# Kernel optimization log

Hardware: AMD Instinct MI355X
Metric: run time of the kernel (lower is better)

The kernel has to match this reference:

```python
import jax, jax.numpy as jnp
import numpy as np

DIM = 16      # sdefunc.dim (latent channels)
S = 64        # spatial side of latent volume
HID = 64      # drift conv hidden channels
DT = 0.05     # sdeint dt
SIGMA = 0.1   # diagonal diffusion coefficient
N_STEPS = 20  # (t1 - t0) / dt with ts = [0, 1]


def conv3d(v, w, b):
    # v: [B, C, D, H, W], w: [O, I, 3, 3, 3]
    y = jax.lax.conv_general_dilated(
        v, w, window_strides=(1, 1, 1), padding='SAME',
        dimension_numbers=('NCDHW', 'OIDHW', 'NCDHW'))
    return y + b[None, :, None, None, None]


def setup_inputs() -> dict:
    key = jax.random.key(0)
    k = jax.random.split(key, 6)
    x = jax.random.normal(k[0], (1, DIM, S, S, S), dtype=jnp.float32)
    integration_time = jnp.arange(2, dtype=jnp.float32)  # ts = [0.0, 1.0]
    # drift network params (Conv3d(DIM->HID) -> tanh -> Conv3d(HID->DIM))
    w1 = jax.random.normal(k[1], (HID, DIM, 3, 3, 3), dtype=jnp.float32) / np.sqrt(DIM * 27)
    b1 = jnp.zeros((HID,), dtype=jnp.float32)
    w2 = jax.random.normal(k[2], (DIM, HID, 3, 3, 3), dtype=jnp.float32) / np.sqrt(HID * 27)
    b2 = jnp.zeros((DIM,), dtype=jnp.float32)
    # pre-sampled standard-normal Brownian increments, one per Euler step
    noise = jax.random.normal(k[3], (N_STEPS, 1, DIM * S * S * S), dtype=jnp.float32)
    return {"x": x, "integration_time": integration_time,
            "w1": w1, "b1": b1, "w2": w2, "b2": b2, "noise": noise}


def reference(x, integration_time, w1, b1, w2, b2, noise):
    B = x.shape[0]  # == 1 (required by the original reshape)
    y0 = x.reshape(B, -1)  # [B, DIM*S^3]
    sqrt_dt = jnp.float32(DT ** 0.5)

    def drift(y):
        v = y.reshape(B, DIM, S, S, S)
        h = jnp.tanh(conv3d(v, w1, b1))
        f = conv3d(h, w2, b2)
        return f.reshape(B, -1)

    def step(y, z):
        # Euler-Maruyama, diagonal noise: y += f(t,y) dt + sigma * sqrt(dt) * z
        y = y + drift(y) * DT + SIGMA * sqrt_dt * z
        return y, None

    yT, _ = jax.lax.scan(step, y0, noise)
    out = yT.reshape(DIM, S, S, S)  # out[-1] of the trajectory (B == 1)
    return out[None]  # [1, DIM, S, S, S]
```

## Files before the change

### kernel.cpp

```cpp
#include <hip/hip_runtime.h>
#include <hip/hip_bf16.h>


#define S    64
#define SS   4096
#define SSS  262144
#define DT_F 0.05f
#define SIG_SDT 0.022360679774997897f

typedef __bf16 bf16x8 __attribute__((ext_vector_type(8)));
typedef float  f32x4  __attribute__((ext_vector_type(4)));
typedef float  f32x16 __attribute__((ext_vector_type(16)));

union B8U { uint4 u; bf16x8 b; };
__device__ inline bf16x8 as_bf16x8(uint4 u) { B8U x; x.u = u; return x.b; }

__device__ inline unsigned short bf16_bits(float f) {
    union { float f; unsigned u; } c; c.f = f;
    unsigned r = c.u + 0x7fffu + ((c.u >> 16) & 1u);
    return (unsigned short)(r >> 16);
}

__device__ inline float tanh_fast(float v) {
    float a = fminf(fmaxf(v, -15.f), 15.f);
    float e = __expf(2.f * a);
    return (e - 1.f) * __builtin_amdgcn_rcpf(e + 1.f);
}

__global__ void prep_weights(const float* __restrict__ w1, const float* __restrict__ w2,
                             unsigned short* __restrict__ w1t, unsigned short* __restrict__ w2t)
{
    const int t = blockIdx.x * 256 + threadIdx.x;
    if (t >= 27 * 2 * 64 * 8) return;
    const int j = t & 7, l = (t >> 3) & 63, half = (t >> 9) & 1, tap = t >> 10;
    {
        const int oc = half * 32 + (l & 31), ic = (l >> 5) * 8 + j;
        w1t[t] = bf16_bits(w1[(oc * 16 + ic) * 27 + tap]);
    }
    {
        const int oc = l & 15, ic = half * 32 + (l >> 4) * 8 + j;
        w2t[t] = bf16_bits(w2[(oc * 64 + ic) * 27 + tap]);
    }
}

__global__ void pack_x(const float* __restrict__ x, uint4* __restrict__ yb)
{
    const int p = blockIdx.x * 256 + threadIdx.x;
    union { unsigned short s[16]; uint4 v[2]; } pk;
    #pragma unroll
    for (int c = 0; c < 16; ++c) pk.s[c] = bf16_bits(x[c * SSS + p]);
    yb[p * 2]     = pk.v[0];
    yb[p * 2 + 1] = pk.v[1];
}

__device__ inline void stage1(const uint4* __restrict__ yb, uint4* tile,
                              int y, int zp, int t)
{
    uint4* dst = tile + ((zp % 3 + 3) % 3) * 396;
    for (int idx = t; idx < 396; idx += 256) {
        const int r = idx / 132, rem = idx - r * 132;
        const int px = rem >> 1;
        const int gy = y + r - 1, gx = px - 1;
        uint4 v = {0, 0, 0, 0};
        if ((unsigned)zp < 64u && (unsigned)gy < 64u && (unsigned)gx < 64u)
            v = yb[(((size_t)zp * SS + gy * S + gx) << 1) + (rem & 1)];
        dst[idx] = v;
    }
}

__global__ __launch_bounds__(256, 2)
void conv1_mfma(const uint4* __restrict__ yb, const uint4* __restrict__ w1t,
                const float* __restrict__ b1, unsigned short* __restrict__ h)
{
    __shared__ uint4 tile[3 * 396];
    const int t = threadIdx.x, lane = t & 63, w = t >> 6;
    const int mt = w >> 1, xg = w & 1;
    const int y = blockIdx.y, z0 = blockIdx.x * 4;

    bf16x8 A[27];
    #pragma unroll
    for (int tap = 0; tap < 27; ++tap)
        A[tap] = as_bf16x8(w1t[(tap * 2 + mt) * 64 + lane]);

    const int n = lane & 31, hh = lane >> 5;
    float bias[16];
    #pragma unroll
    for (int q = 0; q < 4; ++q)
        #pragma unroll
        for (int i = 0; i < 4; ++i)
            bias[q * 4 + i] = b1[mt * 32 + q * 8 + hh * 4 + i];

    stage1(yb, tile, y, z0 - 1, t);
    stage1(yb, tile, y, z0,     t);

    for (int zi = 0; zi < 4; ++zi) {
        const int z = z0 + zi;
        __syncthreads();
        stage1(yb, tile, y, z + 1, t);
        __syncthreads();

        f32x16 acc;
        #pragma unroll
        for (int i = 0; i < 16; ++i) acc[i] = 0.f;

        #pragma unroll
        for (int dz = 0; dz < 3; ++dz) {
            const uint4* pl = tile + (((z - 1 + dz) % 3 + 3) % 3) * 396;
            #pragma unroll
            for (int dy = 0; dy < 3; ++dy) {
                const uint4* row = pl + dy * 132;
                #pragma unroll
                for (int dx = 0; dx < 3; ++dx) {
                    bf16x8 B = as_bf16x8(row[(xg * 32 + n + dx) * 2 + hh]);
                    acc = __builtin_amdgcn_mfma_f32_32x32x16_bf16(
                              A[dz * 9 + dy * 3 + dx], B, acc, 0, 0, 0);
                }
            }
        }

        const int x = xg * 32 + n;
        const size_t p = (size_t)z * SS + y * S + x;
        unsigned short* hp = h + p * 64;
        #pragma unroll
        for (int q = 0; q < 4; ++q) {
            const int oc = mt * 32 + q * 8 + hh * 4;
            union { unsigned short s[4]; uint2 v; } pk;
            #pragma unroll
            for (int i = 0; i < 4; ++i)
                pk.s[i] = bf16_bits(tanh_fast(acc[q * 4 + i] + bias[q * 4 + i]));
            *(uint2*)(hp + oc) = pk.v;
        }
    }
}

__device__ inline void stage2(const uint4* __restrict__ hsrc, uint4* tile,
                              int y, int x0, int zp, int t)
{
    uint4* dst = tile + ((zp % 3 + 3) % 3) * 816;
    for (int idx = t; idx < 816; idx += 256) {
        const int r = idx / 272, rem = idx - r * 272;
        const int px = rem >> 3, c = rem & 7;
        const int gy = y + r - 1, gx = x0 + px - 1;
        uint4 v = {0, 0, 0, 0};
        if ((unsigned)zp < 64u && (unsigned)gy < 64u && (unsigned)gx < 64u)
            v = hsrc[((size_t)zp * SS + gy * S + gx) * 8 + c];
        dst[r * 272 + px * 8 + (c ^ (px & 7))] = v;
    }
}

__global__ __launch_bounds__(256, 3)
void conv2_mfma(const uint4* __restrict__ hsrc, const uint4* __restrict__ w2t,
                const float* __restrict__ b2, const float* __restrict__ ysrc,
                float* __restrict__ ydst, unsigned short* __restrict__ yb,
                const float* __restrict__ nz)
{
    __shared__ uint4 tile[3 * 816];
    __shared__ f32x4 scratch[128];
    const int t = threadIdx.x, lane = t & 63, w = t >> 6;
    const int kc = w >> 1, xg = w & 1;
    const int x0 = blockIdx.x * 32, y = blockIdx.y, z0 = blockIdx.z * 8;

    bf16x8 A[27];
    #pragma unroll
    for (int tap = 0; tap < 27; ++tap)
        A[tap] = as_bf16x8(w2t[(tap * 2 + kc) * 64 + lane]);

    const int n16 = lane & 15, g = lane >> 4;
    float b2v[4];
    #pragma unroll
    for (int i = 0; i < 4; ++i) b2v[i] = b2[g * 4 + i];

    stage2(hsrc, tile, y, x0, z0 - 1, t);
    stage2(hsrc, tile, y, x0, z0,     t);

    for (int zi = 0; zi < 8; ++zi) {
        const int z = z0 + zi;
        __syncthreads();
        stage2(hsrc, tile, y, x0, z + 1, t);
        __syncthreads();

        f32x4 acc = {0.f, 0.f, 0.f, 0.f};
        #pragma unroll
        for (int dz = 0; dz < 3; ++dz) {
            const uint4* pl = tile + (((z - 1 + dz) % 3 + 3) % 3) * 816;
            #pragma unroll
            for (int dy = 0; dy < 3; ++dy) {
                const uint4* row = pl + dy * 272;
                #pragma unroll
                for (int dx = 0; dx < 3; ++dx) {
                    const int px = xg * 16 + n16 + dx;
                    const int c  = kc * 4 + g;
                    bf16x8 B = as_bf16x8(row[px * 8 + (c ^ (px & 7))]);
                    acc = __builtin_amdgcn_mfma_f32_16x16x32_bf16(
                              A[dz * 9 + dy * 3 + dx], B, acc, 0, 0, 0);
                }
            }
        }

        if (kc == 1) scratch[xg * 64 + lane] = acc;
        __syncthreads();
        if (kc == 0) {
            f32x4 o = scratch[xg * 64 + lane];
            const int x = x0 + xg * 16 + n16;
            const size_t p = (size_t)z * SS + y * S + x;
            union { unsigned short s[4]; uint2 v; } pk;
            #pragma unroll
            for (int i = 0; i < 4; ++i) {
                const size_t idx = (size_t)(g * 4 + i) * SSS + p;
                const float f  = acc[i] + o[i] + b2v[i];
                const float yv = ysrc[idx] + f * DT_F + SIG_SDT * nz[idx];
                ydst[idx] = yv;
                pk.s[i] = bf16_bits(yv);
            }
            *(uint2*)(yb + p * 16 + g * 4) = pk.v;
        }
    }
}

extern "C" void kernel_launch(void* const* d_in, const int* in_sizes, int n_in,
                              void* d_out, int out_size, void* d_ws, size_t ws_size,
                              hipStream_t stream)
{
    (void)in_sizes; (void)n_in; (void)out_size; (void)ws_size;
    const float* x     = (const float*)d_in[0];
    const float* w1    = (const float*)d_in[2];
    const float* b1    = (const float*)d_in[3];
    const float* w2    = (const float*)d_in[4];
    const float* b2    = (const float*)d_in[5];
    const float* noise = (const float*)d_in[6];

    char* ws = (char*)d_ws;
    unsigned short* w1t = (unsigned short*)ws;
    unsigned short* w2t = (unsigned short*)(ws + 55296);
    uint4* yb = (uint4*)(ws + 131072);
    uint4* hb = (uint4*)(ws + 131072 + 8388608);
    float* y  = (float*)d_out;

    prep_weights<<<108, 256, 0, stream>>>(w1, w2, w1t, w2t);
    pack_x<<<1024, 256, 0, stream>>>(x, yb);

    for (int s = 0; s < 20; ++s) {
        conv1_mfma<<<dim3(16, 64), 256, 0, stream>>>(
            yb, (const uint4*)w1t, b1, (unsigned short*)hb);
        const float* ys = (s == 0) ? x : (const float*)y;
        conv2_mfma<<<dim3(2, 64, 8), 256, 0, stream>>>(
            hb, (const uint4*)w2t, b2, ys, y, (unsigned short*)yb,
            noise + (size_t)s * (16 * SSS));
    }
}
```

Measured before the change: 2.149 ms.

## Use zero-padded global activations and drop LDS staging in both convs

Stores the bf16 latent and hidden activations in zero-padded 66^3 volumes so halo reads need no bounds checks. Both conv kernels then drop shared-memory tiling and barriers and load B operands directly from global/L2. Each loaded plane is reused across three rotating z accumulators, so every input plane is read once per kernel. Grid and block shapes change (conv1 does 8 z per block, conv2 uses 128-thread blocks over 16-wide x tiles). This adds a zeroing pass over the larger workspace and relies on cache hits for the overlapping halo reads.

```diff
diff --git a/kernel.cpp b/kernel.cpp
--- a/kernel.cpp
+++ b/kernel.cpp
@@ -1,5 +1,4 @@
 #include <hip/hip_runtime.h>
-#include <hip/hip_bf16.h>
 
 
 #define S    64
@@ -7,6 +6,7 @@
 #define SSS  262144
 #define DT_F 0.05f
 #define SIG_SDT 0.022360679774997897f
+#define PD   66
 
 typedef __bf16 bf16x8 __attribute__((ext_vector_type(8)));
 typedef float  f32x4  __attribute__((ext_vector_type(4)));
@@ -25,6 +25,13 @@
     float a = fminf(fmaxf(v, -15.f), 15.f);
     float e = __expf(2.f * a);
     return (e - 1.f) * __builtin_amdgcn_rcpf(e + 1.f);
+}
+
+__global__ void zero_ws(uint4* __restrict__ p, unsigned n)
+{
+    const uint4 z = {0u, 0u, 0u, 0u};
+    for (unsigned i = blockIdx.x * 256u + threadIdx.x; i < n; i += gridDim.x * 256u)
+        p[i] = z;
 }
 
 __global__ void prep_weights(const float* __restrict__ w1, const float* __restrict__ w2,
@@ -43,176 +50,159 @@
     }
 }
 
-__global__ void pack_x(const float* __restrict__ x, uint4* __restrict__ yb)
+__global__ void pack_x(const float* __restrict__ x, char* __restrict__ ybp)
 {
     const int p = blockIdx.x * 256 + threadIdx.x;
+    const int z = p >> 12, yy = (p >> 6) & 63, xx = p & 63;
     union { unsigned short s[16]; uint4 v[2]; } pk;
     #pragma unroll
     for (int c = 0; c < 16; ++c) pk.s[c] = bf16_bits(x[c * SSS + p]);
-    yb[p * 2]     = pk.v[0];
-    yb[p * 2 + 1] = pk.v[1];
-}
-
-__device__ inline void stage1(const uint4* __restrict__ yb, uint4* tile,
-                              int y, int zp, int t)
-{
-    uint4* dst = tile + ((zp % 3 + 3) % 3) * 396;
-    for (int idx = t; idx < 396; idx += 256) {
-        const int r = idx / 132, rem = idx - r * 132;
-        const int px = rem >> 1;
-        const int gy = y + r - 1, gx = px - 1;
-        uint4 v = {0, 0, 0, 0};
-        if ((unsigned)zp < 64u && (unsigned)gy < 64u && (unsigned)gx < 64u)
-            v = yb[(((size_t)zp * SS + gy * S + gx) << 1) + (rem & 1)];
-        dst[idx] = v;
-    }
+    char* dst = ybp + (((size_t)(z + 1) * PD + (yy + 1)) * PD + (xx + 1)) * 32;
+    *(uint4*)dst        = pk.v[0];
+    *(uint4*)(dst + 16) = pk.v[1];
 }
 
 __global__ __launch_bounds__(256, 2)
-void conv1_mfma(const uint4* __restrict__ yb, const uint4* __restrict__ w1t,
-                const float* __restrict__ b1, unsigned short* __restrict__ h)
-{
-    __shared__ uint4 tile[3 * 396];
+void conv1_mfma(const char* __restrict__ ybp, const uint4* __restrict__ w1t,
+                const float* __restrict__ b1, char* __restrict__ hbp)
+{
     const int t = threadIdx.x, lane = t & 63, w = t >> 6;
     const int mt = w >> 1, xg = w & 1;
-    const int y = blockIdx.y, z0 = blockIdx.x * 4;
+    const int y = blockIdx.y, z0 = blockIdx.x * 8;
+    const int n = lane & 31, hh = lane >> 5;
+    const int x0 = xg * 32;
 
     bf16x8 A[27];
     #pragma unroll
     for (int tap = 0; tap < 27; ++tap)
         A[tap] = as_bf16x8(w1t[(tap * 2 + mt) * 64 + lane]);
 
-    const int n = lane & 31, hh = lane >> 5;
     float bias[16];
     #pragma unroll
     for (int q = 0; q < 4; ++q)
         #pragma unroll
-        for (int i = 0; i < 4; ++i)
-            bias[q * 4 + i] = b1[mt * 32 + q * 8 + hh * 4 + i];
-
-    stage1(yb, tile, y, z0 - 1, t);
-    stage1(yb, tile, y, z0,     t);
-
-    for (int zi = 0; zi < 4; ++zi) {
-        const int z = z0 + zi;
-        __syncthreads();
-        stage1(yb, tile, y, z + 1, t);
-        __syncthreads();
-
-        f32x16 acc;
-        #pragma unroll
-        for (int i = 0; i < 16; ++i) acc[i] = 0.f;
-
-        #pragma unroll
-        for (int dz = 0; dz < 3; ++dz) {
-            const uint4* pl = tile + (((z - 1 + dz) % 3 + 3) % 3) * 396;
-            #pragma unroll
-            for (int dy = 0; dy < 3; ++dy) {
-                const uint4* row = pl + dy * 132;
+        for (int j = 0; j < 4; ++j)
+            bias[q * 4 + j] = b1[mt * 32 + q * 8 + hh * 4 + j];
+
+    const char* ybl = ybp + (x0 + n) * 32 + hh * 16;
+    char* hbl = hbp + ((size_t)(y + 1) * PD + (x0 + n + 1)) * 128
+                    + (mt * 32 + hh * 4) * 2;
+
+    f32x16 acc[3];
+    #pragma unroll
+    for (int s = 0; s < 3; ++s)
+        #pragma unroll
+        for (int q = 0; q < 16; ++q) acc[s][q] = 0.f;
+
+    #pragma unroll
+    for (int i = 0; i < 10; ++i) {
+        const int zp = z0 - 1 + i;
+        const char* pb = ybl + ((size_t)(zp + 1) * PD + y) * (PD * 32);
+        #pragma unroll
+        for (int dy = 0; dy < 3; ++dy) {
+            #pragma unroll
+            for (int dx = 0; dx < 3; ++dx) {
+                bf16x8 B = as_bf16x8(*(const uint4*)(pb + (dy * PD + dx) * 32));
+                if (i < 8)
+                    acc[(i + 1) % 3] = __builtin_amdgcn_mfma_f32_32x32x16_bf16(
+                        A[0 + dy * 3 + dx], B, acc[(i + 1) % 3], 0, 0, 0);
+                if (i >= 1 && i <= 8)
+                    acc[i % 3] = __builtin_amdgcn_mfma_f32_32x32x16_bf16(
+                        A[9 + dy * 3 + dx], B, acc[i % 3], 0, 0, 0);
+                if (i >= 2)
+                    acc[(i + 2) % 3] = __builtin_amdgcn_mfma_f32_32x32x16_bf16(
+                        A[18 + dy * 3 + dx], B, acc[(i + 2) % 3], 0, 0, 0);
+            }
+        }
+        if (i >= 2) {
+            const int z = zp - 1;
+            char* hp = hbl + (size_t)(z + 1) * (PD * PD * 128);
+            f32x16 a = acc[(i + 2) % 3];
+            #pragma unroll
+            for (int q = 0; q < 4; ++q) {
+                union { unsigned short sh[4]; uint2 v; } pk;
                 #pragma unroll
-                for (int dx = 0; dx < 3; ++dx) {
-                    bf16x8 B = as_bf16x8(row[(xg * 32 + n + dx) * 2 + hh]);
-                    acc = __builtin_amdgcn_mfma_f32_32x32x16_bf16(
-                              A[dz * 9 + dy * 3 + dx], B, acc, 0, 0, 0);
-                }
-            }
-        }
-
-        const int x = xg * 32 + n;
-        const size_t p = (size_t)z * SS + y * S + x;
-        unsigned short* hp = h + p * 64;
-        #pragma unroll
-        for (int q = 0; q < 4; ++q) {
-            const int oc = mt * 32 + q * 8 + hh * 4;
-            union { unsigned short s[4]; uint2 v; } pk;
-            #pragma unroll
-            for (int i = 0; i < 4; ++i)
-                pk.s[i] = bf16_bits(tanh_fast(acc[q * 4 + i] + bias[q * 4 + i]));
-            *(uint2*)(hp + oc) = pk.v;
-        }
-    }
-}
-
-__device__ inline void stage2(const uint4* __restrict__ hsrc, uint4* tile,
-                              int y, int x0, int zp, int t)
-{
-    uint4* dst = tile + ((zp % 3 + 3) % 3) * 816;
-    for (int idx = t; idx < 816; idx += 256) {
-        const int r = idx / 272, rem = idx - r * 272;
-        const int px = rem >> 3, c = rem & 7;
-        const int gy = y + r - 1, gx = x0 + px - 1;
-        uint4 v = {0, 0, 0, 0};
-        if ((unsigned)zp < 64u && (unsigned)gy < 64u && (unsigned)gx < 64u)
-            v = hsrc[((size_t)zp * SS + gy * S + gx) * 8 + c];
-        dst[r * 272 + px * 8 + (c ^ (px & 7))] = v;
-    }
-}
-
-__global__ __launch_bounds__(256, 3)
-void conv2_mfma(const uint4* __restrict__ hsrc, const uint4* __restrict__ w2t,
+                for (int j = 0; j < 4; ++j)
+                    pk.sh[j] = bf16_bits(tanh_fast(a[q * 4 + j] + bias[q * 4 + j]));
+                *(uint2*)(hp + q * 16) = pk.v;
+            }
+            #pragma unroll
+            for (int q = 0; q < 16; ++q) acc[(i + 2) % 3][q] = 0.f;
+        }
+    }
+}
+
+__global__ __launch_bounds__(128, 3)
+void conv2_mfma(const char* __restrict__ hbp, const uint4* __restrict__ w2t,
                 const float* __restrict__ b2, const float* __restrict__ ysrc,
-                float* __restrict__ ydst, unsigned short* __restrict__ yb,
+                float* __restrict__ ydst, char* __restrict__ ybp,
                 const float* __restrict__ nz)
 {
-    __shared__ uint4 tile[3 * 816];
-    __shared__ f32x4 scratch[128];
-    const int t = threadIdx.x, lane = t & 63, w = t >> 6;
-    const int kc = w >> 1, xg = w & 1;
-    const int x0 = blockIdx.x * 32, y = blockIdx.y, z0 = blockIdx.z * 8;
+    __shared__ f32x4 scratch[2][64];
+    const int t = threadIdx.x, lane = t & 63, kc = t >> 6;
+    const int y = blockIdx.y, z0 = blockIdx.z * 8, x0 = blockIdx.x * 16;
+    const int n16 = lane & 15, g = lane >> 4;
 
     bf16x8 A[27];
     #pragma unroll
     for (int tap = 0; tap < 27; ++tap)
         A[tap] = as_bf16x8(w2t[(tap * 2 + kc) * 64 + lane]);
 
-    const int n16 = lane & 15, g = lane >> 4;
     float b2v[4];
     #pragma unroll
-    for (int i = 0; i < 4; ++i) b2v[i] = b2[g * 4 + i];
-
-    stage2(hsrc, tile, y, x0, z0 - 1, t);
-    stage2(hsrc, tile, y, x0, z0,     t);
-
-    for (int zi = 0; zi < 8; ++zi) {
-        const int z = z0 + zi;
-        __syncthreads();
-        stage2(hsrc, tile, y, x0, z + 1, t);
-        __syncthreads();
-
-        f32x4 acc = {0.f, 0.f, 0.f, 0.f};
-        #pragma unroll
-        for (int dz = 0; dz < 3; ++dz) {
-            const uint4* pl = tile + (((z - 1 + dz) % 3 + 3) % 3) * 816;
-            #pragma unroll
-            for (int dy = 0; dy < 3; ++dy) {
-                const uint4* row = pl + dy * 272;
+    for (int j = 0; j < 4; ++j) b2v[j] = b2[g * 4 + j];
+
+    const char* hbl = hbp + (x0 + n16) * 128 + kc * 64 + g * 16;
+
+    f32x4 acc[3];
+    #pragma unroll
+    for (int s = 0; s < 3; ++s)
+        #pragma unroll
+        for (int q = 0; q < 4; ++q) acc[s][q] = 0.f;
+
+    #pragma unroll
+    for (int i = 0; i < 10; ++i) {
+        const int zp = z0 - 1 + i;
+        const char* pb = hbl + ((size_t)(zp + 1) * PD + y) * (PD * 128);
+        #pragma unroll
+        for (int dy = 0; dy < 3; ++dy) {
+            #pragma unroll
+            for (int dx = 0; dx < 3; ++dx) {
+                bf16x8 B = as_bf16x8(*(const uint4*)(pb + (dy * PD + dx) * 128));
+                if (i < 8)
+                    acc[(i + 1) % 3] = __builtin_amdgcn_mfma_f32_16x16x32_bf16(
+                        A[0 + dy * 3 + dx], B, acc[(i + 1) % 3], 0, 0, 0);
+                if (i >= 1 && i <= 8)
+                    acc[i % 3] = __builtin_amdgcn_mfma_f32_16x16x32_bf16(
+                        A[9 + dy * 3 + dx], B, acc[i % 3], 0, 0, 0);
+                if (i >= 2)
+                    acc[(i + 2) % 3] = __builtin_amdgcn_mfma_f32_16x16x32_bf16(
+                        A[18 + dy * 3 + dx], B, acc[(i + 2) % 3], 0, 0, 0);
+            }
+        }
+        if (i >= 2) {
+            const int z = zp - 1;
+            f32x4 a = acc[(i + 2) % 3];
+            #pragma unroll
+            for (int q = 0; q < 4; ++q) acc[(i + 2) % 3][q] = 0.f;
+            if (kc == 1) scratch[i & 1][lane] = a;
+            __syncthreads();
+            if (kc == 0) {
+                f32x4 o = scratch[i & 1][lane];
+                const size_t p = (size_t)z * SS + y * S + (x0 + n16);
+                union { unsigned short sh[4]; uint2 v; } pk;
                 #pragma unroll
-                for (int dx = 0; dx < 3; ++dx) {
-                    const int px = xg * 16 + n16 + dx;
-                    const int c  = kc * 4 + g;
-                    bf16x8 B = as_bf16x8(row[px * 8 + (c ^ (px & 7))]);
-                    acc = __builtin_amdgcn_mfma_f32_16x16x32_bf16(
-                              A[dz * 9 + dy * 3 + dx], B, acc, 0, 0, 0);
+                for (int j = 0; j < 4; ++j) {
+                    const size_t idx = (size_t)(g * 4 + j) * SSS + p;
+                    const float f  = a[j] + o[j] + b2v[j];
+                    const float yv = ysrc[idx] + f * DT_F + SIG_SDT * nz[idx];
+                    ydst[idx] = yv;
+                    pk.sh[j] = bf16_bits(yv);
                 }
-            }
-        }
-
-        if (kc == 1) scratch[xg * 64 + lane] = acc;
-        __syncthreads();
-        if (kc == 0) {
-            f32x4 o = scratch[xg * 64 + lane];
-            const int x = x0 + xg * 16 + n16;
-            const size_t p = (size_t)z * SS + y * S + x;
-            union { unsigned short s[4]; uint2 v; } pk;
-            #pragma unroll
-            for (int i = 0; i < 4; ++i) {
-                const size_t idx = (size_t)(g * 4 + i) * SSS + p;
-                const float f  = acc[i] + o[i] + b2v[i];
-                const float yv = ysrc[idx] + f * DT_F + SIG_SDT * nz[idx];
-                ydst[idx] = yv;
-                pk.s[i] = bf16_bits(yv);
-            }
-            *(uint2*)(yb + p * 16 + g * 4) = pk.v;
+                char* yb = ybp + (((size_t)(z + 1) * PD + (y + 1)) * PD
+                                  + (x0 + n16 + 1)) * 32 + g * 8;
+                *(uint2*)yb = pk.v;
+            }
         }
     }
 }
@@ -232,19 +222,20 @@
     char* ws = (char*)d_ws;
     unsigned short* w1t = (unsigned short*)ws;
     unsigned short* w2t = (unsigned short*)(ws + 55296);
-    uint4* yb = (uint4*)(ws + 131072);
-    uint4* hb = (uint4*)(ws + 131072 + 8388608);
+    char* ybp = ws + 131072;
+    char* hbp = ws + 131072 + 9199872;
     float* y  = (float*)d_out;
 
+    zero_ws<<<2048, 256, 0, stream>>>((uint4*)ybp, (9199872u + 36799488u) / 16u);
     prep_weights<<<108, 256, 0, stream>>>(w1, w2, w1t, w2t);
-    pack_x<<<1024, 256, 0, stream>>>(x, yb);
+    pack_x<<<1024, 256, 0, stream>>>(x, ybp);
 
     for (int s = 0; s < 20; ++s) {
-        conv1_mfma<<<dim3(16, 64), 256, 0, stream>>>(
-            yb, (const uint4*)w1t, b1, (unsigned short*)hb);
+        conv1_mfma<<<dim3(8, 64), 256, 0, stream>>>(
+            ybp, (const uint4*)w1t, b1, hbp);
         const float* ys = (s == 0) ? x : (const float*)y;
-        conv2_mfma<<<dim3(2, 64, 8), 256, 0, stream>>>(
-            hb, (const uint4*)w2t, b2, ys, y, (unsigned short*)yb,
+        conv2_mfma<<<dim3(4, 64, 8), 128, 0, stream>>>(
+            hbp, (const uint4*)w2t, b2, ys, y, ybp,
             noise + (size_t)s * (16 * SSS));
     }
 }
```

Measured after the change: 2.141 ms. Within noise of the previous version (-0.4%).
